# Performance work log

Measured on AMD Instinct MI355X. Metric: run time of the kernel, lower is better.

## Reference

```python
import jax, jax.numpy as jnp
import numpy as np

GROUPS = 8
EPS = 1e-5


def setup_inputs() -> dict:
    key = jax.random.key(0)
    ks = jax.random.split(key, 5)
    b, c, h, w = 16, 512, 64, 64
    x = jax.random.normal(ks[0], (b, c, h, w), dtype=jnp.float32)
    norm_w = jnp.ones((c,), dtype=jnp.float32)
    norm_b = jnp.zeros((c,), dtype=jnp.float32)
    # 1x1 conv weights stored as [out, in] (kernel spatial dims are 1)
    qkv_w = jax.random.normal(ks[1], (3 * c, c), dtype=jnp.float32) * (c ** -0.5)
    qkv_b = jax.random.normal(ks[2], (3 * c,), dtype=jnp.float32) * 0.02
    proj_w = jax.random.normal(ks[3], (c, c), dtype=jnp.float32) * (c ** -0.5)
    proj_b = jax.random.normal(ks[4], (c,), dtype=jnp.float32) * 0.02
    return {"x": x, "norm_w": norm_w, "norm_b": norm_b,
            "qkv_w": qkv_w, "qkv_b": qkv_b, "proj_w": proj_w, "proj_b": proj_b}


def reference(x, norm_w, norm_b, qkv_w, qkv_b, proj_w, proj_b):
    b, c, h, w = x.shape
    n = h * w
    # GroupNorm over (c/groups, h, w) per group, affine per channel
    xg = x.reshape(b, GROUPS, -1)
    mean = xg.mean(axis=-1, keepdims=True)
    var = xg.var(axis=-1, keepdims=True)
    xn = ((xg - mean) * jax.lax.rsqrt(var + EPS)).reshape(b, c, n)
    xn = xn * norm_w[None, :, None] + norm_b[None, :, None]
    # 1x1 conv qkv: [b, 3c, n]
    qkv = jnp.einsum('oc,bcn->bon', qkv_w, xn) + qkv_b[None, :, None]
    qkv = qkv.reshape(b, 3, c, n)
    q, k, v = qkv[:, 0], qkv[:, 1], qkv[:, 2]  # each [b, c, n]
    scale = jnp.asarray(c, x.dtype) ** -0.5
    # NOTE: as in the source, attention is over channels: attn is [b, c, c]
    attn = jnp.einsum('bcn,bdn->bcd', q, k) * scale
    attn = jax.nn.softmax(attn, axis=-1)
    out = jnp.einsum('bcd,bdn->bcn', attn, v)  # [b, c, n]
    out = jnp.einsum('oc,bcn->bon', proj_w, out) + proj_b[None, :, None]
    return x + out.reshape(b, c, h, w)
```

## Files before the change

kernel.cpp:

```cpp
#include <hip/hip_runtime.h>
#include <hip/hip_bf16.h>

using bf16 = __hip_bfloat16;
typedef __attribute__((ext_vector_type(8))) short short8;
typedef __attribute__((ext_vector_type(4))) float f32x4;
typedef __attribute__((ext_vector_type(4))) short short4v;

#define B_   16
#define C_   512
#define N_   4096
#define NG   8
#define GRP_ELEMS (64 * 4096)
static constexpr float kScale = 0.04419417382415922f;
#define SPART_STRIDE 4194304ULL

#define OFF_WQ    0ULL
#define OFF_WP    0x180000ULL
#define OFF_STATS 0x200000ULL
#define OFF_PART  0x204000ULL
#define OFF_SUM   0x210000ULL
#define OFF_U     0x220000ULL
#define OFF_W     0x230000ULL
#define OFF_WVT   0x240000ULL
#define OFF_BV2   0x2C0000ULL
#define OFF_Q     0x400000ULL
#define OFF_K     (OFF_Q  + 0x4000000ULL)
#define OFF_VT    (OFF_K  + 0x4000000ULL)
#define OFF_XNC   OFF_Q
#define OFF_G2    OFF_Q
#define OFF_P     (OFF_Q + 0x1000000ULL)
#define OFF_ATT   (OFF_Q + 0x2000000ULL)
#define OFF_GP    OFF_K
#define OFF_W2    OFF_K
#define OFF_W3    (OFF_K + 0x800000ULL)

typedef __attribute__((address_space(1))) const void* as1cvp;
typedef __attribute__((address_space(3))) void* as3vp;

__device__ inline void gload_lds16(const void* g, void* l) {
  __builtin_amdgcn_global_load_lds((as1cvp)g, (as3vp)l, 16, 0, 0);
}

#define BARX() __builtin_amdgcn_s_barrier()
#define SFEN() __builtin_amdgcn_sched_barrier(0)
#define LG0()  asm volatile("s_waitcnt lgkmcnt(0)" ::: "memory")
#define VM4()  asm volatile("s_waitcnt vmcnt(4)" ::: "memory")
#define VM0()  asm volatile("s_waitcnt vmcnt(0)" ::: "memory")

__global__ __launch_bounds__(256) void cvt_weights(const float* __restrict__ wq,
                                                   const float* __restrict__ wp,
                                                   bf16* __restrict__ oq,
                                                   bf16* __restrict__ op,
                                                   bf16* __restrict__ wvt) {
  int i = blockIdx.x * 256 + threadIdx.x;
  if (i < 1536 * 512) oq[i] = __float2bfloat16(wq[i]);
  if (i < 512 * 512) {
    op[i] = __float2bfloat16(wp[i]);
    const int d = i >> 9, c = i & 511;
    wvt[c * 512 + d] = __float2bfloat16(wq[(1024 + d) * 512 + c]);
  }
}

__global__ __launch_bounds__(256) void gn_stats_part(const float* __restrict__ x,
                                                     float* __restrict__ part) {
  const int bg  = blockIdx.x >> 4;
  const int seg = blockIdx.x & 15;
  const float4* p = (const float4*)(x + (size_t)bg * GRP_ELEMS + seg * 16384);
  float s = 0.f, q = 0.f;
#pragma unroll
  for (int i = 0; i < 16; ++i) {
    float4 v = p[threadIdx.x + i * 256];
    s += v.x + v.y + v.z + v.w;
    q += v.x * v.x + v.y * v.y + v.z * v.z + v.w * v.w;
  }
  for (int off = 32; off; off >>= 1) { s += __shfl_xor(s, off); q += __shfl_xor(q, off); }
  __shared__ float red[8];
  int w = threadIdx.x >> 6;
  if ((threadIdx.x & 63) == 0) { red[w] = s; red[4 + w] = q; }
  __syncthreads();
  if (threadIdx.x == 0) {
    part[blockIdx.x * 2]     = red[0] + red[1] + red[2] + red[3];
    part[blockIdx.x * 2 + 1] = red[4] + red[5] + red[6] + red[7];
  }
}

__global__ __launch_bounds__(128) void gn_stats_fin(const float* __restrict__ part,
                                                    float* __restrict__ stats) {
  const int bg = threadIdx.x;
  float S = 0.f, Q = 0.f;
#pragma unroll
  for (int i = 0; i < 16; ++i) {
    S += part[(bg * 16 + i) * 2];
    Q += part[(bg * 16 + i) * 2 + 1];
  }
  const float mean = S * (1.f / GRP_ELEMS);
  const float var  = Q * (1.f / GRP_ELEMS) - mean * mean;
  stats[bg * 2]     = mean;
  stats[bg * 2 + 1] = rsqrtf(var + 1e-5f);
}

__global__ __launch_bounds__(256) void gn_apply_t(const float* __restrict__ x,
                                                  const float* __restrict__ stats,
                                                  const float* __restrict__ nw,
                                                  const float* __restrict__ nb,
                                                  bf16* __restrict__ xnt,
                                                  bf16* __restrict__ xncn) {
  const int nt = blockIdx.x;
  const int ct = blockIdx.y;
  const int b  = blockIdx.z;
  __shared__ float tile[64][65];
  const float mean = stats[(b * NG + ct) * 2];
  const float rstd = stats[(b * NG + ct) * 2 + 1];
  const int col = threadIdx.x & 63;
  const int r4  = threadIdx.x >> 6;
#pragma unroll
  for (int p = 0; p < 16; ++p) {
    int cl = p * 4 + r4;
    int c  = ct * 64 + cl;
    float g  = nw[c] * rstd;
    float sh = nb[c] - mean * g;
    float v  = x[((size_t)b * C_ + c) * N_ + nt * 64 + col];
    float xv = v * g + sh;
    tile[cl][col] = xv;
    xncn[((size_t)b * C_ + c) * N_ + nt * 64 + col] = __float2bfloat16(xv);
  }
  __syncthreads();
#pragma unroll
  for (int p = 0; p < 16; ++p) {
    int nl = p * 4 + r4;
    xnt[((size_t)b * N_ + nt * 64 + nl) * C_ + ct * 64 + col] =
        __float2bfloat16(tile[col][nl]);
  }
}

__global__ __launch_bounds__(256) void sums_xn(const bf16* __restrict__ xncn,
                                               float* __restrict__ s) {
  const int b = blockIdx.x >> 7, ct = blockIdx.x & 127;
  const int w = threadIdx.x >> 6, l = threadIdx.x & 63;
  const int c = ct * 4 + w;
  const bf16* row = xncn + ((size_t)b * C_ + c) * N_;
  float acc = 0.f;
  for (int k = 0; k < 8; ++k) {
    short8 v8 = *(const short8*)(row + k * 512 + l * 8);
#pragma unroll
    for (int i = 0; i < 8; ++i) {
      short t = v8[i];
      acc += __bfloat162float(*reinterpret_cast<const bf16*>(&t));
    }
  }
  for (int off = 32; off; off >>= 1) acc += __shfl_xor(acc, off);
  if (l == 0) s[b * C_ + c] = acc;
}

__global__ __launch_bounds__(256) void greduce(const float* __restrict__ gp,
                                               bf16* __restrict__ g2) {
  const size_t base = ((size_t)blockIdx.x * 256 + threadIdx.x) * 8;
  float g[8];
#pragma unroll
  for (int j = 0; j < 8; ++j)
    g[j] = gp[base + j] + gp[SPART_STRIDE + base + j] +
           gp[2 * SPART_STRIDE + base + j] + gp[3 * SPART_STRIDE + base + j];
  const int b = (int)(base >> 18), rem = (int)(base & 262143);
  const int e = rem >> 9, k = rem & 511;
  bf16* hi = g2 + ((size_t)b * 512 + e) * 1024 + k;
#pragma unroll
  for (int j = 0; j < 8; ++j) {
    bf16 h = __float2bfloat16(g[j]);
    hi[j]       = h;
    hi[512 + j] = __float2bfloat16(g[j] - __bfloat162float(h));
  }
}

__global__ __launch_bounds__(512) void gemv_uw(const float* __restrict__ qw,
                                               const float* __restrict__ s,
                                               float* __restrict__ u,
                                               float* __restrict__ w) {
  const int b = blockIdx.x >> 1, which = blockIdx.x & 1;
  const int c = threadIdx.x;
  const float* row = qw + (size_t)(which * 512 + c) * 512;
  const float* sv = s + b * 512;
  float acc = 0.f;
  for (int d = 0; d < 512; d += 4) {
    float4 wv = *(const float4*)(row + d);
    float4 s4 = *(const float4*)(sv + d);
    acc += wv.x * s4.x + wv.y * s4.y + wv.z * s4.z + wv.w * s4.w;
  }
  (which ? w : u)[b * 512 + c] = acc;
}

__global__ __launch_bounds__(512) void gemv_bv2(const bf16* __restrict__ w2,
                                                const float* __restrict__ qkv_b,
                                                const float* __restrict__ proj_b,
                                                float* __restrict__ bias2) {
  const int b = blockIdx.x, o = threadIdx.x;
  const bf16* row = w2 + (size_t)b * 262144 + o * 512;
  float acc = proj_b[o];
  for (int d = 0; d < 512; d += 8) {
    short8 v8 = *(const short8*)(row + d);
#pragma unroll
    for (int i = 0; i < 8; ++i) {
      short t = v8[i];
      acc += __bfloat162float(*reinterpret_cast<const bf16*>(&t)) *
             qkv_b[1024 + d + i];
    }
  }
  bias2[b * 512 + o] = acc;
}

template<int MODE>
__global__ __launch_bounds__(512, 2) void gemm8p(
    const bf16* __restrict__ Ag, const bf16* __restrict__ Bg,
    int lda, int ldb, long long sA, long long sB,
    const float* __restrict__ bias,
    void* __restrict__ o0, void* __restrict__ o1, void* __restrict__ o2,
    const float* __restrict__ resid) {
  __shared__ __align__(16) bf16 smem[8][8192];

  constexpr int NIT = (MODE == 1 || MODE == 4) ? 8 : 4;
  const int id = blockIdx.x;
  int bx, by, bz, part;
  if constexpr (MODE == 1) {
    const int s = (id & 7) * 32 + (id >> 3);
    bx = s & 1; by = (s >> 1) & 1; part = (s >> 2) & 3; bz = s >> 4;
  } else if constexpr (MODE == 3) {
    const int s = (id & 7) * 64 + (id >> 3);
    by = s & 1;  bx = (s >> 1) & 15;  bz = s >> 5; part = 0;
  } else {
    const int s = (id & 7) * 8 + (id >> 3);
    bx = s & 1;  by = (s >> 1) & 1;  bz = s >> 2; part = 0;
  }

  const bf16* Apan = Ag + (size_t)bz * sA + (size_t)by * 256 * lda + (size_t)part * 1024;
  const bf16* Bpan = Bg + (size_t)bz * sB + (size_t)bx * 256 * ldb + (size_t)part * 1024;

  const int tid  = threadIdx.x;
  const int lane = tid & 63;
  const int wid  = tid >> 6;
  const int wr   = wid >> 2;
  const int wc   = wid & 3;
  const int mrow = lane & 15, krow = lane >> 4;
  const int wrr  = wr * 64, wcc = wc * 32;

  auto stage = [&](int mat, int buf, int half, int kt) {
    const int ktp = (MODE == 4 && mat == 0) ? (kt & 7) : kt;
    const bf16* gb = mat ? Bpan : Apan;
    const int ld = mat ? ldb : lda;
    char* reg = (char*)smem[mat * 4 + buf * 2 + half];
#pragma unroll
    for (int j = 0; j < 2; ++j) {
      const int idx = j * 512 + tid;
      const int r   = idx >> 3;
      const int c8  = (tid & 7) ^ (r & 7);
      gload_lds16(gb + (size_t)(half * 128 + r) * ld + ktp * 64 + c8 * 8,
                  reg + idx * 16);
    }
  };

  short8 a[4][2], b0[2][2], b1[2][2];
  auto ldA = [&](int buf, int qm) {
    const char* reg = (const char*)smem[buf * 2 + qm];
#pragma unroll
    for (int mi = 0; mi < 4; ++mi) {
      const int lr = wrr + mi * 16 + mrow;
#pragma unroll
      for (int s2 = 0; s2 < 2; ++s2)
        a[mi][s2] = *(const short8*)(reg + lr * 128 +
                                     (((s2 * 4 + krow) ^ (lr & 7)) << 4));
    }
  };
  auto ldB = [&](short8 (&b)[2][2], int buf, int qn) {
    const char* reg = (const char*)smem[4 + buf * 2 + qn];
#pragma unroll
    for (int ni = 0; ni < 2; ++ni) {
      const int lr = wcc + ni * 16 + mrow;
#pragma unroll
      for (int s2 = 0; s2 < 2; ++s2)
        b[ni][s2] = *(const short8*)(reg + lr * 128 +
                                     (((s2 * 4 + krow) ^ (lr & 7)) << 4));
    }
  };

  f32x4 acc[2][2][4][2];
#pragma unroll
  for (int p = 0; p < 2; ++p)
#pragma unroll
    for (int q = 0; q < 2; ++q)
#pragma unroll
      for (int m = 0; m < 4; ++m)
#pragma unroll
        for (int n = 0; n < 2; ++n)
#pragma unroll
          for (int r = 0; r < 4; ++r) acc[p][q][m][n][r] = 0.f;

  auto mm = [&](short8 (&b)[2][2], f32x4 (&c)[4][2]) {
    __builtin_amdgcn_s_setprio(1);
#pragma unroll
    for (int mi = 0; mi < 4; ++mi)
#pragma unroll
      for (int ni = 0; ni < 2; ++ni)
#pragma unroll
        for (int s2 = 0; s2 < 2; ++s2)
          c[mi][ni] = __builtin_amdgcn_mfma_f32_16x16x32_bf16(
              a[mi][s2], b[ni][s2], c[mi][ni], 0, 0, 0);
    __builtin_amdgcn_s_setprio(0);
  };

  stage(0, 0, 0, 0); stage(0, 0, 1, 0); stage(1, 0, 0, 0); stage(1, 0, 1, 0);
  stage(0, 1, 0, 1); stage(1, 1, 0, 1);
  VM4(); BARX(); SFEN();

  for (int i = 0; i < NIT; ++i) {
    const int kt1 = 2 * i + 1, kt2 = 2 * i + 2, kt3 = 2 * i + 3;
    const bool more = (i < NIT - 1);
    ldA(0, 0); ldB(b0, 0, 0); stage(0, 1, 1, kt1);
    BARX(); LG0(); SFEN(); mm(b0, acc[0][0]); BARX();
    ldB(b1, 0, 1); stage(1, 1, 1, kt1);
    BARX(); LG0(); SFEN(); mm(b1, acc[0][1]); BARX();
    ldA(0, 1); if (more) stage(0, 0, 0, kt2);
    BARX(); LG0(); SFEN(); mm(b0, acc[1][0]); BARX();
    if (more) { stage(1, 0, 0, kt2); VM4(); } else { VM0(); }
    BARX(); SFEN(); mm(b1, acc[1][1]); BARX();
    ldA(1, 0); ldB(b0, 1, 0); if (more) stage(0, 0, 1, kt2);
    BARX(); LG0(); SFEN(); mm(b0, acc[0][0]); BARX();
    ldB(b1, 1, 1); if (more) stage(1, 0, 1, kt2);
    BARX(); LG0(); SFEN(); mm(b1, acc[0][1]); BARX();
    ldA(1, 1); if (more) stage(0, 1, 0, kt3);
    BARX(); LG0(); SFEN(); mm(b0, acc[1][0]); BARX();
    if (more) { stage(1, 1, 0, kt3); VM4(); }
    BARX(); SFEN(); mm(b1, acc[1][1]);
    if (more) BARX();
  }

#pragma unroll
  for (int qm = 0; qm < 2; ++qm)
#pragma unroll
  for (int qn = 0; qn < 2; ++qn)
#pragma unroll
  for (int mi = 0; mi < 4; ++mi)
#pragma unroll
  for (int ni = 0; ni < 2; ++ni)
#pragma unroll
  for (int rr = 0; rr < 4; ++rr) {
    const int row_l = qm * 128 + wrr + mi * 16 + krow * 4 + rr;
    const int col_l = qn * 128 + wcc + ni * 16 + mrow;
    float v = acc[qm][qn][mi][ni][rr];
    if constexpr (MODE == 1) {
      const int row = by * 256 + row_l, colg = bx * 256 + col_l;
      ((float*)o0)[(size_t)part * SPART_STRIDE + (size_t)bz * 262144 +
                   row * 512 + colg] = v;
    } else if constexpr (MODE == 2) {
      const int o = by * 256 + row_l, d = bx * 256 + col_l;
      ((bf16*)o0)[(size_t)bz * 262144 + o * 512 + d] = __float2bfloat16(v);
    } else if constexpr (MODE == 3) {
      const int o = by * 256 + row_l;
      const int n = bx * 256 + col_l;
      const size_t addr = ((size_t)bz * C_ + o) * N_ + n;
      ((float*)o0)[addr] = v + bias[(bz << 9) + o] + resid[addr];
    } else if constexpr (MODE == 4) {
      const int c = by * 256 + row_l, e = bx * 256 + col_l;
      ((bf16*)o0)[(size_t)bz * 262144 + c * 512 + e] = __float2bfloat16(v);
    } else {
      const int row = by * 256 + row_l, col = bx * 256 + col_l;
      const float* uu = (const float*)o1;
      const float* ww = (const float*)o2;
      const float bq = bias[row], bk = bias[512 + col];
      const float corr = uu[bz * 512 + row] * bk + bq * ww[bz * 512 + col] +
                         4096.f * bq * bk;
      ((float*)o0)[(size_t)bz * 262144 + row * 512 + col] = (v + corr) * kScale;
    }
  }
}

__global__ __launch_bounds__(256) void softmax_t(const float* __restrict__ S,
                                                 bf16* __restrict__ att_t) {
  const int b  = blockIdx.x >> 3;
  const int ct = blockIdx.x & 7;
  __shared__ bf16 T[512][68];
  const int w = threadIdx.x >> 6, lane = threadIdx.x & 63;
  for (int it = 0; it < 16; ++it) {
    const int cl  = w * 16 + it;
    const int row = b * 512 + ct * 64 + cl;
    const float* p = S + (size_t)row * 512;
    float v[8];
    float mx = -1e30f;
#pragma unroll
    for (int i = 0; i < 8; ++i) { v[i] = p[lane + i * 64]; mx = fmaxf(mx, v[i]); }
    for (int off = 32; off; off >>= 1) mx = fmaxf(mx, __shfl_xor(mx, off));
    float s = 0.f;
#pragma unroll
    for (int i = 0; i < 8; ++i) { v[i] = __expf(v[i] - mx); s += v[i]; }
    for (int off = 32; off; off >>= 1) s += __shfl_xor(s, off);
    float inv = 1.f / s;
#pragma unroll
    for (int i = 0; i < 8; ++i) T[lane + i * 64][cl] = __float2bfloat16(v[i] * inv);
  }
  __syncthreads();
  bf16* outp = att_t + (size_t)b * 262144 + ct * 64;
  const int dof = threadIdx.x >> 4;
  const int c4  = (threadIdx.x & 15) * 4;
  for (int it = 0; it < 32; ++it) {
    const int d = it * 16 + dof;
    *(short4v*)(outp + (size_t)d * 512 + c4) = *(const short4v*)(&T[d][c4]);
  }
}

extern "C" void kernel_launch(void* const* d_in, const int* in_sizes, int n_in,
                              void* d_out, int out_size, void* d_ws, size_t ws_size,
                              hipStream_t stream) {
  const float* x      = (const float*)d_in[0];
  const float* norm_w = (const float*)d_in[1];
  const float* norm_b = (const float*)d_in[2];
  const float* qkv_w  = (const float*)d_in[3];
  const float* qkv_b  = (const float*)d_in[4];
  const float* proj_w = (const float*)d_in[5];
  const float* proj_b = (const float*)d_in[6];
  float* out = (float*)d_out;
  char* ws = (char*)d_ws;

  bf16*  wq    = (bf16*)(ws + OFF_WQ);
  bf16*  wp    = (bf16*)(ws + OFF_WP);
  bf16*  wvt   = (bf16*)(ws + OFF_WVT);
  float* stats = (float*)(ws + OFF_STATS);
  float* partb = (float*)(ws + OFF_PART);
  float* ssum  = (float*)(ws + OFF_SUM);
  float* u     = (float*)(ws + OFF_U);
  float* wv_   = (float*)(ws + OFF_W);
  float* bias2 = (float*)(ws + OFF_BV2);
  bf16*  xncn  = (bf16*)(ws + OFF_XNC);
  bf16*  g2    = (bf16*)(ws + OFF_G2);
  bf16*  P     = (bf16*)(ws + OFF_P);
  bf16*  att_t = (bf16*)(ws + OFF_ATT);
  float* gpart = (float*)(ws + OFF_GP);
  bf16*  w2    = (bf16*)(ws + OFF_W2);
  bf16*  w3    = (bf16*)(ws + OFF_W3);
  bf16*  xnt   = (bf16*)(ws + OFF_VT);
  float* S     = (float*)d_out;

  cvt_weights<<<3072, 256, 0, stream>>>(qkv_w, proj_w, wq, wp, wvt);
  gn_stats_part<<<2048, 256, 0, stream>>>(x, partb);
  gn_stats_fin<<<1, 128, 0, stream>>>(partb, stats);
  gn_apply_t<<<dim3(64, 8, 16), 256, 0, stream>>>(x, stats, norm_w, norm_b,
                                                  xnt, xncn);
  gemm8p<1><<<256, 512, 0, stream>>>(xncn, xncn, 4096, 4096, 2097152LL,
                                     2097152LL, nullptr, gpart, nullptr,
                                     nullptr, nullptr);
  sums_xn<<<2048, 256, 0, stream>>>(xncn, ssum);
  greduce<<<2048, 256, 0, stream>>>(gpart, g2);
  gemv_uw<<<32, 512, 0, stream>>>(qkv_w, ssum, u, wv_);
  gemm8p<4><<<64, 512, 0, stream>>>(wq, g2, 512, 1024, 0, 524288LL,
                                    nullptr, P, nullptr, nullptr, nullptr);
  gemm8p<5><<<64, 512, 0, stream>>>(P, wq + 512 * 512, 512, 512, 262144LL, 0,
                                    qkv_b, S, u, wv_, nullptr);
  softmax_t<<<128, 256, 0, stream>>>(S, att_t);
  gemm8p<2><<<64, 512, 0, stream>>>(wp, att_t, 512, 512, 0, 262144LL,
                                    nullptr, w2, nullptr, nullptr, nullptr);
  gemm8p<2><<<64, 512, 0, stream>>>(w2, wvt, 512, 512, 262144LL, 0,
                                    nullptr, w3, nullptr, nullptr, nullptr);
  gemv_bv2<<<16, 512, 0, stream>>>(w2, qkv_b, proj_b, bias2);
  gemm8p<3><<<512, 512, 0, stream>>>(w3, xnt, 512, 512, 262144LL, 2097152LL,
                                     bias2, out, nullptr, nullptr, x);
}
```

Before: 419.1 us.

## Fuse prep kernels, atomically reduce split-K Gram, fold channel sums into GN apply

Merges weight conversion with the GroupNorm partial-statistics pass into one launch, and finalizes the statistics inside gn_apply_t, which also accumulates per-channel sums of the normalized activations with atomics. This removes the separate stats-finalize and sums_xn kernels. The split-K Gram GEMM now atomically adds into a single zeroed buffer instead of writing four partial slices, so greduce becomes a plain convert. Softmax uses 256 smaller blocks for more parallelism. The cost is two memsets, a float-atomic write pattern in the GEMM epilogue that is nondeterministic in order, and channel sums taken from fp32 rather than from the bf16-rounded values.

Result: slower. 501.4 us (+19.6%).

```diff
diff --git a/kernel.cpp b/kernel.cpp
--- a/kernel.cpp
+++ b/kernel.cpp
@@ -12,7 +12,6 @@
 #define NG   8
 #define GRP_ELEMS (64 * 4096)
 static constexpr float kScale = 0.04419417382415922f;
-#define SPART_STRIDE 4194304ULL
 
 #define OFF_WQ    0ULL
 #define OFF_WP    0x180000ULL
@@ -30,7 +29,7 @@
 #define OFF_G2    OFF_Q
 #define OFF_P     (OFF_Q + 0x1000000ULL)
 #define OFF_ATT   (OFF_Q + 0x2000000ULL)
-#define OFF_GP    OFF_K
+#define OFF_G     OFF_K
 #define OFF_W2    OFF_K
 #define OFF_W3    (OFF_K + 0x800000ULL)
 
@@ -47,24 +46,26 @@
 #define VM4()  asm volatile("s_waitcnt vmcnt(4)" ::: "memory")
 #define VM0()  asm volatile("s_waitcnt vmcnt(0)" ::: "memory")
 
-__global__ __launch_bounds__(256) void cvt_weights(const float* __restrict__ wq,
-                                                   const float* __restrict__ wp,
-                                                   bf16* __restrict__ oq,
-                                                   bf16* __restrict__ op,
-                                                   bf16* __restrict__ wvt) {
-  int i = blockIdx.x * 256 + threadIdx.x;
-  if (i < 1536 * 512) oq[i] = __float2bfloat16(wq[i]);
-  if (i < 512 * 512) {
-    op[i] = __float2bfloat16(wp[i]);
-    const int d = i >> 9, c = i & 511;
-    wvt[c * 512 + d] = __float2bfloat16(wq[(1024 + d) * 512 + c]);
-  }
-}
-
-__global__ __launch_bounds__(256) void gn_stats_part(const float* __restrict__ x,
-                                                     float* __restrict__ part) {
-  const int bg  = blockIdx.x >> 4;
-  const int seg = blockIdx.x & 15;
+__global__ __launch_bounds__(256) void prep(const float* __restrict__ wq,
+                                            const float* __restrict__ wp,
+                                            const float* __restrict__ x,
+                                            bf16* __restrict__ oq,
+                                            bf16* __restrict__ op,
+                                            bf16* __restrict__ wvt,
+                                            float* __restrict__ part) {
+  if (blockIdx.x < 3072) {
+    int i = blockIdx.x * 256 + threadIdx.x;
+    oq[i] = __float2bfloat16(wq[i]);
+    if (i < 512 * 512) {
+      op[i] = __float2bfloat16(wp[i]);
+      const int d = i >> 9, c = i & 511;
+      wvt[c * 512 + d] = __float2bfloat16(wq[(1024 + d) * 512 + c]);
+    }
+    return;
+  }
+  const int bid = blockIdx.x - 3072;
+  const int bg  = bid >> 4;
+  const int seg = bid & 15;
   const float4* p = (const float4*)(x + (size_t)bg * GRP_ELEMS + seg * 16384);
   float s = 0.f, q = 0.f;
 #pragma unroll
@@ -79,38 +80,33 @@
   if ((threadIdx.x & 63) == 0) { red[w] = s; red[4 + w] = q; }
   __syncthreads();
   if (threadIdx.x == 0) {
-    part[blockIdx.x * 2]     = red[0] + red[1] + red[2] + red[3];
-    part[blockIdx.x * 2 + 1] = red[4] + red[5] + red[6] + red[7];
-  }
-}
-
-__global__ __launch_bounds__(128) void gn_stats_fin(const float* __restrict__ part,
-                                                    float* __restrict__ stats) {
-  const int bg = threadIdx.x;
-  float S = 0.f, Q = 0.f;
-#pragma unroll
-  for (int i = 0; i < 16; ++i) {
-    S += part[(bg * 16 + i) * 2];
-    Q += part[(bg * 16 + i) * 2 + 1];
-  }
-  const float mean = S * (1.f / GRP_ELEMS);
-  const float var  = Q * (1.f / GRP_ELEMS) - mean * mean;
-  stats[bg * 2]     = mean;
-  stats[bg * 2 + 1] = rsqrtf(var + 1e-5f);
+    part[bid * 2]     = red[0] + red[1] + red[2] + red[3];
+    part[bid * 2 + 1] = red[4] + red[5] + red[6] + red[7];
+  }
 }
 
 __global__ __launch_bounds__(256) void gn_apply_t(const float* __restrict__ x,
-                                                  const float* __restrict__ stats,
+                                                  const float* __restrict__ part,
                                                   const float* __restrict__ nw,
                                                   const float* __restrict__ nb,
                                                   bf16* __restrict__ xnt,
-                                                  bf16* __restrict__ xncn) {
+                                                  bf16* __restrict__ xncn,
+                                                  float* __restrict__ ssum) {
   const int nt = blockIdx.x;
   const int ct = blockIdx.y;
   const int b  = blockIdx.z;
   __shared__ float tile[64][65];
-  const float mean = stats[(b * NG + ct) * 2];
-  const float rstd = stats[(b * NG + ct) * 2 + 1];
+  const int bg = b * NG + ct;
+  float Sm = 0.f, Qm = 0.f;
+#pragma unroll
+  for (int i = 0; i < 16; ++i) {
+    Sm += part[(bg * 16 + i) * 2];
+    Qm += part[(bg * 16 + i) * 2 + 1];
+  }
+  const float mean = Sm * (1.f / GRP_ELEMS);
+  const float var  = Qm * (1.f / GRP_ELEMS) - mean * mean;
+  const float rstd = rsqrtf(var + 1e-5f);
+
   const int col = threadIdx.x & 63;
   const int r4  = threadIdx.x >> 6;
 #pragma unroll
@@ -123,6 +119,9 @@
     float xv = v * g + sh;
     tile[cl][col] = xv;
     xncn[((size_t)b * C_ + c) * N_ + nt * 64 + col] = __float2bfloat16(xv);
+    float ws_ = xv;
+    for (int off = 32; off; off >>= 1) ws_ += __shfl_xor(ws_, off);
+    if (col == 0) atomicAdd(&ssum[b * C_ + c], ws_);
   }
   __syncthreads();
 #pragma unroll
@@ -133,41 +132,18 @@
   }
 }
 
-__global__ __launch_bounds__(256) void sums_xn(const bf16* __restrict__ xncn,
-                                               float* __restrict__ s) {
-  const int b = blockIdx.x >> 7, ct = blockIdx.x & 127;
-  const int w = threadIdx.x >> 6, l = threadIdx.x & 63;
-  const int c = ct * 4 + w;
-  const bf16* row = xncn + ((size_t)b * C_ + c) * N_;
-  float acc = 0.f;
-  for (int k = 0; k < 8; ++k) {
-    short8 v8 = *(const short8*)(row + k * 512 + l * 8);
-#pragma unroll
-    for (int i = 0; i < 8; ++i) {
-      short t = v8[i];
-      acc += __bfloat162float(*reinterpret_cast<const bf16*>(&t));
-    }
-  }
-  for (int off = 32; off; off >>= 1) acc += __shfl_xor(acc, off);
-  if (l == 0) s[b * C_ + c] = acc;
-}
-
-__global__ __launch_bounds__(256) void greduce(const float* __restrict__ gp,
-                                               bf16* __restrict__ g2) {
+__global__ __launch_bounds__(256) void g2cvt(const float* __restrict__ G,
+                                             bf16* __restrict__ g2) {
   const size_t base = ((size_t)blockIdx.x * 256 + threadIdx.x) * 8;
-  float g[8];
-#pragma unroll
-  for (int j = 0; j < 8; ++j)
-    g[j] = gp[base + j] + gp[SPART_STRIDE + base + j] +
-           gp[2 * SPART_STRIDE + base + j] + gp[3 * SPART_STRIDE + base + j];
   const int b = (int)(base >> 18), rem = (int)(base & 262143);
   const int e = rem >> 9, k = rem & 511;
   bf16* hi = g2 + ((size_t)b * 512 + e) * 1024 + k;
 #pragma unroll
   for (int j = 0; j < 8; ++j) {
-    bf16 h = __float2bfloat16(g[j]);
+    float g = G[base + j];
+    bf16 h = __float2bfloat16(g);
     hi[j]       = h;
-    hi[512 + j] = __float2bfloat16(g[j] - __bfloat162float(h));
+    hi[512 + j] = __float2bfloat16(g - __bfloat162float(h));
   }
 }
 
@@ -346,8 +322,7 @@
     float v = acc[qm][qn][mi][ni][rr];
     if constexpr (MODE == 1) {
       const int row = by * 256 + row_l, colg = bx * 256 + col_l;
-      ((float*)o0)[(size_t)part * SPART_STRIDE + (size_t)bz * 262144 +
-                   row * 512 + colg] = v;
+      atomicAdd(&((float*)o0)[(size_t)bz * 262144 + row * 512 + colg], v);
     } else if constexpr (MODE == 2) {
       const int o = by * 256 + row_l, d = bx * 256 + col_l;
       ((bf16*)o0)[(size_t)bz * 262144 + o * 512 + d] = __float2bfloat16(v);
@@ -373,13 +348,13 @@
 
 __global__ __launch_bounds__(256) void softmax_t(const float* __restrict__ S,
                                                  bf16* __restrict__ att_t) {
-  const int b  = blockIdx.x >> 3;
-  const int ct = blockIdx.x & 7;
-  __shared__ bf16 T[512][68];
+  const int b  = blockIdx.x >> 4;
+  const int ct = blockIdx.x & 15;
+  __shared__ bf16 T[512][36];
   const int w = threadIdx.x >> 6, lane = threadIdx.x & 63;
-  for (int it = 0; it < 16; ++it) {
-    const int cl  = w * 16 + it;
-    const int row = b * 512 + ct * 64 + cl;
+  for (int it = 0; it < 8; ++it) {
+    const int cl  = w * 8 + it;
+    const int row = b * 512 + ct * 32 + cl;
     const float* p = S + (size_t)row * 512;
     float v[8];
     float mx = -1e30f;
@@ -395,11 +370,11 @@
     for (int i = 0; i < 8; ++i) T[lane + i * 64][cl] = __float2bfloat16(v[i] * inv);
   }
   __syncthreads();
-  bf16* outp = att_t + (size_t)b * 262144 + ct * 64;
-  const int dof = threadIdx.x >> 4;
-  const int c4  = (threadIdx.x & 15) * 4;
-  for (int it = 0; it < 32; ++it) {
-    const int d = it * 16 + dof;
+  bf16* outp = att_t + (size_t)b * 262144 + ct * 32;
+  const int dof = threadIdx.x >> 3;
+  const int c4  = (threadIdx.x & 7) * 4;
+  for (int it = 0; it < 16; ++it) {
+    const int d = it * 32 + dof;
     *(short4v*)(outp + (size_t)d * 512 + c4) = *(const short4v*)(&T[d][c4]);
   }
 }
@@ -420,7 +395,6 @@
   bf16*  wq    = (bf16*)(ws + OFF_WQ);
   bf16*  wp    = (bf16*)(ws + OFF_WP);
   bf16*  wvt   = (bf16*)(ws + OFF_WVT);
-  float* stats = (float*)(ws + OFF_STATS);
   float* partb = (float*)(ws + OFF_PART);
   float* ssum  = (float*)(ws + OFF_SUM);
   float* u     = (float*)(ws + OFF_U);
@@ -430,28 +404,27 @@
   bf16*  g2    = (bf16*)(ws + OFF_G2);
   bf16*  P     = (bf16*)(ws + OFF_P);
   bf16*  att_t = (bf16*)(ws + OFF_ATT);
-  float* gpart = (float*)(ws + OFF_GP);
+  float* G     = (float*)(ws + OFF_G);
   bf16*  w2    = (bf16*)(ws + OFF_W2);
   bf16*  w3    = (bf16*)(ws + OFF_W3);
   bf16*  xnt   = (bf16*)(ws + OFF_VT);
   float* S     = (float*)d_out;
 
-  cvt_weights<<<3072, 256, 0, stream>>>(qkv_w, proj_w, wq, wp, wvt);
-  gn_stats_part<<<2048, 256, 0, stream>>>(x, partb);
-  gn_stats_fin<<<1, 128, 0, stream>>>(partb, stats);
-  gn_apply_t<<<dim3(64, 8, 16), 256, 0, stream>>>(x, stats, norm_w, norm_b,
-                                                  xnt, xncn);
+  hipMemsetAsync(G, 0, 16 * 1024 * 1024, stream);
+  hipMemsetAsync(ssum, 0, 16 * 512 * sizeof(float), stream);
+  prep<<<5120, 256, 0, stream>>>(qkv_w, proj_w, x, wq, wp, wvt, partb);
+  gn_apply_t<<<dim3(64, 8, 16), 256, 0, stream>>>(x, partb, norm_w, norm_b,
+                                                  xnt, xncn, ssum);
   gemm8p<1><<<256, 512, 0, stream>>>(xncn, xncn, 4096, 4096, 2097152LL,
-                                     2097152LL, nullptr, gpart, nullptr,
+                                     2097152LL, nullptr, G, nullptr,
                                      nullptr, nullptr);
-  sums_xn<<<2048, 256, 0, stream>>>(xncn, ssum);
-  greduce<<<2048, 256, 0, stream>>>(gpart, g2);
+  g2cvt<<<2048, 256, 0, stream>>>(G, g2);
   gemv_uw<<<32, 512, 0, stream>>>(qkv_w, ssum, u, wv_);
   gemm8p<4><<<64, 512, 0, stream>>>(wq, g2, 512, 1024, 0, 524288LL,
                                     nullptr, P, nullptr, nullptr, nullptr);
   gemm8p<5><<<64, 512, 0, stream>>>(P, wq + 512 * 512, 512, 512, 262144LL, 0,
                                     qkv_b, S, u, wv_, nullptr);
-  softmax_t<<<128, 256, 0, stream>>>(S, att_t);
+  softmax_t<<<256, 256, 0, stream>>>(S, att_t);
   gemm8p<2><<<64, 512, 0, stream>>>(wp, att_t, 512, 512, 0, 262144LL,
                                     nullptr, w2, nullptr, nullptr, nullptr);
   gemm8p<2><<<64, 512, 0, stream>>>(w2, wvt, 512, 512, 262144LL, 0,
```
